# Kernel optimization log

Measured on AMD Instinct MI355X. Metric: run time of the kernel, lower is better.

The kernel has to match this reference:

```python
import jax, jax.numpy as jnp
import numpy as np


def _mlp2(x, W1, b1, W2, b2):
    # Linear -> (BN=identity in eval) -> ReLU -> Linear  (on_last=False: no act on last)
    return jax.nn.relu(x @ W1 + b1) @ W2 + b2


def _layer(x, ef, row, col, pos, p):
    N, Dn = x.shape
    E, De = ef.shape
    (qW, qB, kW, kB, vW, vB, dW1, dB1, dW2, dB2, eW1, eB1, eW2, eB2,
     attW1, attB1, attW2, attB2, nW1, nB1, nW2, nB2, aW, aB) = p
    d_ep = attW2.shape[0]
    H = De // d_ep
    temp = jnp.sqrt(jnp.asarray(d_ep, x.dtype))
    # ---- reverse-edge lookup: for edge (i,j), find edge (j,i) if present ----
    keys = row.astype(jnp.int64) * N + col.astype(jnp.int64)
    rkeys = col.astype(jnp.int64) * N + row.astype(jnp.int64)
    order = jnp.argsort(keys)
    sk = keys[order]
    loc = jnp.clip(jnp.searchsorted(sk, rkeys), 0, E - 1)
    found = sk[loc] == rkeys
    rev = jnp.where(found[:, None], ef[order[loc]], 0.0)  # [E, De]
    # ---- distance mask ----
    diff = pos[row] - pos[col]                              # [E,3]
    dist = jnp.linalg.norm(diff, axis=1, keepdims=True)     # [E,1]
    dfeat = jnp.concatenate([diff, dist], axis=1)           # [E,4]
    dm = jax.nn.sigmoid(_mlp2(dfeat, dW1, dB1, dW2, dB2))[:, 0]  # [E]
    # ---- message ----
    x_i = x[row]
    x_j = x[col]
    upd_edge = _mlp2(jnp.concatenate([x_i, ef, rev, x_j], axis=1), eW1, eB1, eW2, eB2)  # [E,De]
    q = (x_i @ qW + qB).reshape(E, Dn // H, H)              # [E, d_np, H]
    k = (ef @ kW + kB).reshape(E, d_ep, H)                  # [E, d_ep, H]
    v = x_j @ vW + vB                                       # [E, Da]
    h = jnp.concatenate([q, k], axis=1)                     # [E, d_np+d_ep, H]
    h1 = jax.nn.relu(jnp.einsum('ech,oc->eoh', h, attW1) + attB1[None, :, None])
    att = jnp.einsum('ech,oc->eoh', h1, attW2) + attB2[None, :, None]  # [E, d_ep, H]
    att = att * dm[:, None, None]
    prob = jax.nn.softmax(att / temp, axis=1)               # softmax over channel dim
    wv = prob.reshape(E, -1) * v                            # [E, Da]
    # ---- aggregate (scatter max over source node) ----
    agg = jax.ops.segment_max(wv, row, num_segments=N)
    agg = jnp.where(jnp.isneginf(agg), 0.0, agg)
    # ---- node update ----
    upd_node = _mlp2(jnp.concatenate([x, agg], axis=1), nW1, nB1, nW2, nB2)  # [N,Dn]
    # ---- twin-edge attention (mean of updated edges over out/in edges) ----
    ones = jnp.ones((E,), x.dtype)
    dout = jnp.maximum(jax.ops.segment_sum(ones, row, num_segments=N), 1.0)
    din = jnp.maximum(jax.ops.segment_sum(ones, col, num_segments=N), 1.0)
    outf = jax.ops.segment_sum(upd_edge, row, num_segments=N) / dout[:, None]
    incf = jax.ops.segment_sum(upd_edge, col, num_segments=N) / din[:, None]
    eatt = jax.nn.sigmoid(jnp.concatenate([outf, incf], axis=1) @ aW + aB)  # [N,De]
    final = jax.nn.relu(upd_node) * eatt
    return final, upd_edge, prob


def setup_inputs() -> dict:
    N, E, Dn, De, Da, H, L = 10000, 160000, 128, 128, 128, 8, 2
    d_np, d_ep = Dn // H, De // H
    rng = np.random.default_rng(0)
    half = E // 2
    r = rng.integers(0, N, half)
    c = rng.integers(0, N, half)
    edges = jnp.asarray(np.stack([np.concatenate([r, c]), np.concatenate([c, r])]), dtype=jnp.int32)
    ks = iter(jax.random.split(jax.random.key(0), 40))
    def p(*shape, s=0.02):
        return jax.random.normal(next(ks), shape, jnp.float32) * s
    return dict(
        node_feature=p(N, Dn, s=1.0),
        edge_feature=p(E, De, s=1.0),
        edges_indices=edges,
        descriptor=p(N, 8, s=1.0),
        qW=p(L, Dn, Dn), qB=p(L, Dn),
        kW=p(L, De, De), kB=p(L, De),
        vW=p(L, Dn, Da), vB=p(L, Da),
        dW1=p(L, 4, 32), dB1=p(L, 32),
        dW2=p(L, 32, 1), dB2=p(L, 1),
        eW1=p(L, 2 * Dn + 2 * De, Dn + 2 * De), eB1=p(L, Dn + 2 * De),
        eW2=p(L, Dn + 2 * De, De), eB2=p(L, De),
        attW1=p(L, d_np + d_ep, d_np + d_ep), attB1=p(L, d_np + d_ep),
        attW2=p(L, d_ep, d_np + d_ep), attB2=p(L, d_ep),
        nW1=p(L, Dn + Da, Dn + De), nB1=p(L, Dn + De),
        nW2=p(L, Dn + De, Dn), nB2=p(L, Dn),
        aW=p(L, 2 * De, De), aB=p(L, De),
    )


def reference(node_feature, edge_feature, edges_indices, descriptor,
              qW, qB, kW, kB, vW, vB, dW1, dB1, dW2, dB2,
              eW1, eB1, eW2, eB2, attW1, attB1, attW2, attB2,
              nW1, nB1, nW2, nB2, aW, aB):
    row, col = edges_indices[0], edges_indices[1]
    pos = descriptor[:, :3]
    L = qW.shape[0]
    x, ef = node_feature, edge_feature
    probs = []
    for l in range(L):
        p = (qW[l], qB[l], kW[l], kB[l], vW[l], vB[l], dW1[l], dB1[l], dW2[l], dB2[l],
             eW1[l], eB1[l], eW2[l], eB2[l], attW1[l], attB1[l], attW2[l], attB2[l],
             nW1[l], nB1[l], nW2[l], nB2[l], aW[l], aB[l])
        x, ef, prob = _layer(x, ef, row, col, pos, p)
        if l < L - 1 or L == 1:
            x = jax.nn.relu(x)
            ef = jax.nn.relu(ef)
        probs.append(prob)
    return x, ef, jnp.stack(probs)
```

## Files before the change

kernel.cpp:

```cpp
#include <hip/hip_runtime.h>
#include <math.h>

#define HS 524288
#define HSM (HS - 1)
#define ENC_NEGINF 0x007FFFFFu

__device__ __forceinline__ unsigned encf(float f) {
    unsigned b = __float_as_uint(f);
    return (b & 0x80000000u) ? ~b : (b | 0x80000000u);
}
__device__ __forceinline__ float decf(unsigned u) {
    return __uint_as_float((u & 0x80000000u) ? (u & 0x7FFFFFFFu) : ~u);
}

__device__ __forceinline__ unsigned short f2bf(float x) {
    unsigned u = __float_as_uint(x);
    unsigned r = u + 0x7FFFu + ((u >> 16) & 1u);
    return (unsigned short)(r >> 16);
}
__device__ __forceinline__ float bf2f(unsigned short h) {
    return __uint_as_float(((unsigned)h) << 16);
}


__global__ __launch_bounds__(256) void k_init_static(unsigned* hashK, int* hashV,
                                                     int* rowcnt, int* colcnt, int N) {
    int i = blockIdx.x * 256 + threadIdx.x;
    if (i < HS) { hashK[i] = 0xFFFFFFFFu; hashV[i] = 0x7FFFFFFF; }
    if (i < N) { rowcnt[i] = 0; colcnt[i] = 0; }
}

__global__ __launch_bounds__(256) void k_hash_insert(const int* __restrict__ row,
                                                     const int* __restrict__ col,
                                                     unsigned* hashK, int* hashV, int N, int E) {
    int e = blockIdx.x * 256 + threadIdx.x;
    if (e >= E) return;
    unsigned key = (unsigned)row[e] * (unsigned)N + (unsigned)col[e];
    unsigned h = (key * 2654435761u) >> 13; h &= HSM;
    while (true) {
        unsigned prev = atomicCAS(&hashK[h], 0xFFFFFFFFu, key);
        if (prev == 0xFFFFFFFFu || prev == key) { atomicMin(&hashV[h], e); break; }
        h = (h + 1) & HSM;
    }
}

__global__ __launch_bounds__(256) void k_hash_lookup(const int* __restrict__ row,
                                                     const int* __restrict__ col,
                                                     const unsigned* __restrict__ hashK,
                                                     const int* __restrict__ hashV,
                                                     int* __restrict__ ridx,
                                                     int* rowcnt, int* colcnt, int N, int E) {
    int e = blockIdx.x * 256 + threadIdx.x;
    if (e >= E) return;
    int r = row[e], c = col[e];
    unsigned rkey = (unsigned)c * (unsigned)N + (unsigned)r;
    unsigned h = (rkey * 2654435761u) >> 13; h &= HSM;
    int res = -1;
    while (true) {
        unsigned kk = hashK[h];
        if (kk == rkey) { res = hashV[h]; break; }
        if (kk == 0xFFFFFFFFu) break;
        h = (h + 1) & HSM;
    }
    ridx[e] = res;
    atomicAdd(&rowcnt[r], 1);
    atomicAdd(&colcnt[c], 1);
}

__global__ __launch_bounds__(256) void k_layer_init(unsigned* aggenc, float* outf, float* incf, int NC) {
    int i = blockIdx.x * 256 + threadIdx.x;
    if (i >= NC) return;
    aggenc[i] = ENC_NEGINF;
    outf[i] = 0.f;
    incf[i] = 0.f;
}

__global__ __launch_bounds__(256) void k_prep_wt(const float* __restrict__ src,
                                                 unsigned short* __restrict__ whi,
                                                 unsigned short* __restrict__ wlo,
                                                 int K, int Nn) {
    int idx = blockIdx.x * 256 + threadIdx.x;
    if (idx >= K * Nn) return;
    int k = idx / Nn, n = idx - k * Nn;
    float v = src[idx];
    unsigned short h = f2bf(v);
    float hf = bf2f(h);
    unsigned short l = f2bf(v - hf);
    whi[(size_t)n * K + k] = h;
    wlo[(size_t)n * K + k] = l;
}

template <int ACT>
__global__ __launch_bounds__(256) void k_gemm(const float* __restrict__ A,
                                              const float* __restrict__ B,
                                              const float* __restrict__ bias,
                                              float* __restrict__ C,
                                              int M, int Nd, int K, int lda, int ldb, int ldc) {
    __shared__ float As[16][64];
    __shared__ float Bs[16][64];
    const int tid = threadIdx.x;
    const int bm = blockIdx.y * 64, bn = blockIdx.x * 64;
    const int tx = tid & 15, ty = tid >> 4;
    const int mload = tid >> 2, k4 = (tid & 3) << 2;
    const int kload = tid >> 4, n4 = (tid & 15) << 2;
    float acc[4][4] = {};
    const int gmload = bm + mload;
    const bool avalid = (gmload < M);
    const float* aptr = A + (size_t)(avalid ? gmload : (M - 1)) * lda + k4;
    const float* bptr = B + (size_t)kload * ldb + bn + n4;
    for (int kb = 0; kb < K; kb += 16) {
        float4 av = avalid ? *(const float4*)(aptr + kb) : make_float4(0.f, 0.f, 0.f, 0.f);
        As[k4 + 0][mload] = av.x; As[k4 + 1][mload] = av.y;
        As[k4 + 2][mload] = av.z; As[k4 + 3][mload] = av.w;
        *(float4*)&Bs[kload][n4] = *(const float4*)(bptr + (size_t)kb * ldb);
        __syncthreads();
#pragma unroll
        for (int k = 0; k < 16; ++k) {
            float4 a = *(const float4*)&As[k][ty << 2];
            float4 b = *(const float4*)&Bs[k][tx << 2];
            acc[0][0] += a.x * b.x; acc[0][1] += a.x * b.y; acc[0][2] += a.x * b.z; acc[0][3] += a.x * b.w;
            acc[1][0] += a.y * b.x; acc[1][1] += a.y * b.y; acc[1][2] += a.y * b.z; acc[1][3] += a.y * b.w;
            acc[2][0] += a.z * b.x; acc[2][1] += a.z * b.y; acc[2][2] += a.z * b.z; acc[2][3] += a.z * b.w;
            acc[3][0] += a.w * b.x; acc[3][1] += a.w * b.y; acc[3][2] += a.w * b.z; acc[3][3] += a.w * b.w;
        }
        __syncthreads();
    }
#pragma unroll
    for (int i = 0; i < 4; ++i) {
        int gm = bm + (ty << 2) + i;
        if (gm >= M) continue;
        float* crow = C + (size_t)gm * ldc;
#pragma unroll
        for (int j = 0; j < 4; ++j) {
            int gn = bn + (tx << 2) + j;
            float v = acc[i][j];
            if (bias) v += bias[gn];
            if (ACT == 1) v = fmaxf(v, 0.f);
            if (ACT == 2) v = 1.f / (1.f + __expf(-v));
            crow[gn] = v;
        }
    }
}


#define LDP 40

using bfrag = __attribute__((ext_vector_type(8))) short;
using ffrag = __attribute__((ext_vector_type(4))) float;

template <int MODE, int KSTEPS>
__global__ __launch_bounds__(256) void k_mfma_gemm(const float* __restrict__ Asrc,
                                                   const int* __restrict__ ridx,
                                                   const unsigned short* __restrict__ Bhi,
                                                   const unsigned short* __restrict__ Blo,
                                                   const float* __restrict__ bias,
                                                   const float* __restrict__ xa,
                                                   const float* __restrict__ xb,
                                                   const int* __restrict__ rowArr,
                                                   const int* __restrict__ colArr,
                                                   float* __restrict__ outC,
                                                   float* __restrict__ outf,
                                                   float* __restrict__ incf,
                                                   int edgeBase, int Mrows, int reluOut) {
    constexpr int K = KSTEPS * 32;
    __shared__ unsigned short Ah[128 * LDP];
    __shared__ unsigned short Al[128 * LDP];
    __shared__ unsigned short Bh[128 * LDP];
    __shared__ unsigned short Bl[128 * LDP];

    const int tid = threadIdx.x;
    const int bm = blockIdx.y * 128;
    const int bx = blockIdx.x;

    const int sr = tid >> 1;
    const int kh = (tid & 1) * 16;

    const float* p0;
    const float* p1 = nullptr;
    {
        int rc = min(bm + sr, Mrows - 1);
        if (MODE == 0) {
            int e = edgeBase + rc;
            p0 = Asrc + (size_t)e * 128;
            int rv = ridx[e];
            p1 = (rv >= 0) ? (Asrc + (size_t)rv * 128) : nullptr;
        } else if (MODE == 1) {
            p0 = Asrc + (size_t)rc * 384;
        } else {
            p0 = Asrc + (size_t)rc * 128;
        }
    }
    const unsigned short* bhp = Bhi + (size_t)(bx * 128 + sr) * K + kh;
    const unsigned short* blp = Blo + (size_t)(bx * 128 + sr) * K + kh;

    const int wid = tid >> 6;
    const int lane = tid & 63;
    const int wr0 = (wid >> 1) * 64;
    const int wc0 = (wid & 1) * 64;
    const int lm = lane & 15;
    const int lk = (lane >> 4) * 8;

    ffrag acc[4][4];
#pragma unroll
    for (int i = 0; i < 4; ++i)
#pragma unroll
        for (int j = 0; j < 4; ++j)
            acc[i][j] = (ffrag){0.f, 0.f, 0.f, 0.f};

    unsigned short* AhW = &Ah[sr * LDP + kh];
    unsigned short* AlW = &Al[sr * LDP + kh];
    unsigned short* BhW = &Bh[sr * LDP + kh];
    unsigned short* BlW = &Bl[sr * LDP + kh];

    for (int ks = 0; ks < KSTEPS; ++ks) {
        const int kb = ks * 32;
        const float* ap;
        if (MODE == 0) ap = (kb < 128) ? (p0 + kb) : (p1 ? p1 + (kb - 128) : nullptr);
        else ap = p0 + kb;
#pragma unroll
        for (int c = 0; c < 4; ++c) {
            float4 f = ap ? *(const float4*)(ap + kh + c * 4) : make_float4(0.f, 0.f, 0.f, 0.f);
            ushort4 h, l;
            h.x = f2bf(f.x); l.x = f2bf(f.x - bf2f(h.x));
            h.y = f2bf(f.y); l.y = f2bf(f.y - bf2f(h.y));
            h.z = f2bf(f.z); l.z = f2bf(f.z - bf2f(h.z));
            h.w = f2bf(f.w); l.w = f2bf(f.w - bf2f(h.w));
            *(ushort4*)(AhW + c * 4) = h;
            *(ushort4*)(AlW + c * 4) = l;
        }
        {
            uint4 b0 = *(const uint4*)(bhp + kb);
            uint4 b1 = *(const uint4*)(bhp + kb + 8);
            uint4 c0 = *(const uint4*)(blp + kb);
            uint4 c1 = *(const uint4*)(blp + kb + 8);
            *(uint4*)(BhW) = b0; *(uint4*)(BhW + 8) = b1;
            *(uint4*)(BlW) = c0; *(uint4*)(BlW + 8) = c1;
        }
        __syncthreads();
        bfrag a_h[4], a_l[4], b_h[4], b_l[4];
#pragma unroll
        for (int mt = 0; mt < 4; ++mt) {
            int base = (wr0 + mt * 16 + lm) * LDP + lk;
            a_h[mt] = *(const bfrag*)&Ah[base];
            a_l[mt] = *(const bfrag*)&Al[base];
        }
#pragma unroll
        for (int nt = 0; nt < 4; ++nt) {
            int base = (wc0 + nt * 16 + lm) * LDP + lk;
            b_h[nt] = *(const bfrag*)&Bh[base];
            b_l[nt] = *(const bfrag*)&Bl[base];
        }
#pragma unroll
        for (int mt = 0; mt < 4; ++mt)
#pragma unroll
            for (int nt = 0; nt < 4; ++nt) {
                acc[mt][nt] = __builtin_amdgcn_mfma_f32_16x16x32_bf16(a_h[mt], b_h[nt], acc[mt][nt], 0, 0, 0);
                acc[mt][nt] = __builtin_amdgcn_mfma_f32_16x16x32_bf16(a_l[mt], b_h[nt], acc[mt][nt], 0, 0, 0);
                acc[mt][nt] = __builtin_amdgcn_mfma_f32_16x16x32_bf16(a_h[mt], b_l[nt], acc[mt][nt], 0, 0, 0);
            }
        __syncthreads();
    }

    float bv[4];
#pragma unroll
    for (int nt = 0; nt < 4; ++nt) bv[nt] = bias[bx * 128 + wc0 + nt * 16 + lm];

#pragma unroll
    for (int mt = 0; mt < 4; ++mt) {
#pragma unroll
        for (int i = 0; i < 4; ++i) {
            int grow = bm + wr0 + mt * 16 + (lane >> 4) * 4 + i;
            if (grow >= Mrows) continue;
            if (MODE == 0) {
                int e = edgeBase + grow;
                size_t re = (size_t)rowArr[e] * 384;
                size_t ce = (size_t)colArr[e] * 384;
                float* crow = outC + (size_t)grow * 384;
#pragma unroll
                for (int nt = 0; nt < 4; ++nt) {
                    int gcol = bx * 128 + wc0 + nt * 16 + lm;
                    float v = acc[mt][nt][i] + bv[nt] + xa[re + gcol] + xb[ce + gcol];
                    crow[gcol] = fmaxf(v, 0.f);
                }
            } else if (MODE == 1) {
                int e = edgeBase + grow;
                size_t re = (size_t)rowArr[e] * 128;
                size_t ce = (size_t)colArr[e] * 128;
                float* crow = outC + (size_t)e * 128;
#pragma unroll
                for (int nt = 0; nt < 4; ++nt) {
                    int gcol = wc0 + nt * 16 + lm;
                    float v = acc[mt][nt][i] + bv[nt];
                    atomicAdd(&outf[re + gcol], v);
                    atomicAdd(&incf[ce + gcol], v);
                    crow[gcol] = reluOut ? fmaxf(v, 0.f) : v;
                }
            } else {
                float* crow = outC + (size_t)grow * 128;
#pragma unroll
                for (int nt = 0; nt < 4; ++nt) {
                    int gcol = wc0 + nt * 16 + lm;
                    crow[gcol] = acc[mt][nt][i] + bv[nt];
                }
            }
        }
    }
}


__global__ __launch_bounds__(256) void k_attn(const float* __restrict__ xq,
                                              const float* __restrict__ kbuf,
                                              const float* __restrict__ xv,
                                              const float* __restrict__ desc,
                                              const int* __restrict__ row,
                                              const int* __restrict__ col,
                                              const float* __restrict__ attW1,
                                              const float* __restrict__ attB1,
                                              const float* __restrict__ attW2,
                                              const float* __restrict__ attB2,
                                              const float* __restrict__ dW1,
                                              const float* __restrict__ dB1,
                                              const float* __restrict__ dW2,
                                              const float* __restrict__ dB2,
                                              float* __restrict__ prob_out,
                                              unsigned* __restrict__ aggenc, int E) {
    __shared__ float w1t[32 * 36];
    __shared__ float w2t[32 * 18];
    __shared__ float sdw1[128];
    __shared__ float sQ[4][128];
    __shared__ float sK[4][128];
    __shared__ float sV[4][128];
    __shared__ float sP[4][128];
    for (int i = threadIdx.x; i < 1024; i += 256) {
        int o = i >> 5, c = i & 31;
        w1t[c * 36 + o] = attW1[i];
    }
    for (int i = threadIdx.x; i < 512; i += 256) {
        int o = i >> 5, c = i & 31;
        w2t[c * 18 + o] = attW2[i];
    }
    for (int i = threadIdx.x; i < 128; i += 256) sdw1[i] = dW1[i];
    __syncthreads();

    const int wv = threadIdx.x >> 6;
    const int lane = threadIdx.x & 63;
    const int hd = lane & 7;
    const int og = lane >> 3;
    const int c32 = lane & 31;
    const int nw = (gridDim.x * 256) >> 6;
    const int wid = (blockIdx.x * 256 + threadIdx.x) >> 6;

    float* myQ = sQ[wv];
    float* myK = sK[wv];
    float* myV = sV[wv];
    float* myP = sP[wv];

    const float b1_0 = attB1[og * 4 + 0], b1_1 = attB1[og * 4 + 1];
    const float b1_2 = attB1[og * 4 + 2], b1_3 = attB1[og * 4 + 3];
    const float b2_0 = attB2[og * 2 + 0], b2_1 = attB2[og * 2 + 1];
    const float db2v = dB2[0];
    const float dw2v = dW2[c32];
    const float db1v = dB1[c32];

    for (int e0 = wid; e0 < E; e0 += nw) {
        const int e = __builtin_amdgcn_readfirstlane(e0);
        const int r = row[e], cl = col[e];
        float2 qv = *(const float2*)(xq + (size_t)r * 128 + lane * 2);
        float2 kv = *(const float2*)(kbuf + (size_t)e * 128 + lane * 2);
        float2 vv = *(const float2*)(xv + (size_t)cl * 128 + lane * 2);
        *(float2*)(myQ + lane * 2) = qv;
        *(float2*)(myK + lane * 2) = kv;
        *(float2*)(myV + lane * 2) = vv;
        __builtin_amdgcn_wave_barrier();

        float dx = desc[r * 8 + 0] - desc[cl * 8 + 0];
        float dy = desc[r * 8 + 1] - desc[cl * 8 + 1];
        float dz = desc[r * 8 + 2] - desc[cl * 8 + 2];
        float dist = sqrtf(dx * dx + dy * dy + dz * dz);
        float t = db1v + dx * sdw1[c32] + dy * sdw1[32 + c32] + dz * sdw1[64 + c32] + dist * sdw1[96 + c32];
        t = fmaxf(t, 0.f) * dw2v;
        t += __shfl_xor(t, 1, 64); t += __shfl_xor(t, 2, 64); t += __shfl_xor(t, 4, 64);
        t += __shfl_xor(t, 8, 64); t += __shfl_xor(t, 16, 64);
        float dm = 1.f / (1.f + __expf(-(t + db2v)));

        float h0 = b1_0, h1v = b1_1, h2 = b1_2, h3 = b1_3;
#pragma unroll
        for (int ci = 0; ci < 16; ++ci) {
            float hv = myQ[ci * 8 + hd];
            const float4 w = *(const float4*)&w1t[ci * 36 + og * 4];
            h0 += hv * w.x; h1v += hv * w.y; h2 += hv * w.z; h3 += hv * w.w;
        }
#pragma unroll
        for (int ci = 0; ci < 16; ++ci) {
            float hv = myK[ci * 8 + hd];
            const float4 w = *(const float4*)&w1t[(16 + ci) * 36 + og * 4];
            h0 += hv * w.x; h1v += hv * w.y; h2 += hv * w.z; h3 += hv * w.w;
        }
        float hreg[4];
        hreg[0] = fmaxf(h0, 0.f); hreg[1] = fmaxf(h1v, 0.f);
        hreg[2] = fmaxf(h2, 0.f); hreg[3] = fmaxf(h3, 0.f);

        float a0 = b2_0, a1 = b2_1;
#pragma unroll
        for (int c = 0; c < 32; ++c) {
            int src = (c >> 2) * 8 + hd;
            float hv = __shfl(hreg[c & 3], src, 64);
            const float2 w = *(const float2*)&w2t[c * 18 + og * 2];
            a0 += hv * w.x; a1 += hv * w.y;
        }
        float sc = dm * 0.25f;
        a0 *= sc; a1 *= sc;

        float mx = fmaxf(a0, a1);
        mx = fmaxf(mx, __shfl_xor(mx, 8, 64));
        mx = fmaxf(mx, __shfl_xor(mx, 16, 64));
        mx = fmaxf(mx, __shfl_xor(mx, 32, 64));
        float e0v = __expf(a0 - mx), e1v = __expf(a1 - mx);
        float s = e0v + e1v;
        s += __shfl_xor(s, 8, 64); s += __shfl_xor(s, 16, 64); s += __shfl_xor(s, 32, 64);
        float inv = 1.f / s;
        float p0 = e0v * inv, p1 = e1v * inv;

        myP[og * 16 + hd] = p0;
        myP[og * 16 + hd + 8] = p1;

        float v0 = myV[og * 16 + hd] * p0;
        float v1 = myV[og * 16 + hd + 8] * p1;
        unsigned* ab = aggenc + (size_t)r * 128 + og * 16 + hd;
        atomicMax(ab, encf(v0));
        atomicMax(ab + 8, encf(v1));

        __builtin_amdgcn_wave_barrier();
        *(float2*)(prob_out + (size_t)e * 128 + lane * 2) = *(const float2*)(myP + lane * 2);
    }
}


__global__ __launch_bounds__(256) void k_ncat(const float* __restrict__ x,
                                              const unsigned* __restrict__ aggenc,
                                              float* __restrict__ ncat, int N) {
    int i = blockIdx.x * 256 + threadIdx.x;
    if (i >= N * 256) return;
    int n = i >> 8, c = i & 255;
    float v;
    if (c < 128) v = x[n * 128 + c];
    else {
        unsigned u = aggenc[n * 128 + c - 128];
        v = (u == ENC_NEGINF) ? 0.f : decf(u);
    }
    ncat[i] = v;
}

__global__ __launch_bounds__(256) void k_cat2(const float* __restrict__ outf,
                                              const float* __restrict__ incf,
                                              const int* __restrict__ rowcnt,
                                              const int* __restrict__ colcnt,
                                              float* __restrict__ cat2, int N) {
    int i = blockIdx.x * 256 + threadIdx.x;
    if (i >= N * 256) return;
    int n = i >> 8, c = i & 255;
    float v;
    if (c < 128) v = outf[n * 128 + c] / fmaxf((float)rowcnt[n], 1.f);
    else v = incf[n * 128 + c - 128] / fmaxf((float)colcnt[n], 1.f);
    cat2[i] = v;
}

__global__ __launch_bounds__(256) void k_final(const float* __restrict__ un,
                                               const float* __restrict__ eatt,
                                               float* __restrict__ dst, int NC) {
    int i = blockIdx.x * 256 + threadIdx.x;
    if (i >= NC) return;
    dst[i] = fmaxf(un[i], 0.f) * eatt[i];
}


extern "C" void kernel_launch(void* const* d_in, const int* in_sizes, int n_in,
                              void* d_out, int out_size, void* d_ws, size_t ws_size,
                              hipStream_t stream) {
    const float* node_feature = (const float*)d_in[0];
    const float* edge_feature = (const float*)d_in[1];
    const int* edges = (const int*)d_in[2];
    const float* desc = (const float*)d_in[3];
    const float* qW = (const float*)d_in[4];
    const float* qB = (const float*)d_in[5];
    const float* kW = (const float*)d_in[6];
    const float* kB = (const float*)d_in[7];
    const float* vW = (const float*)d_in[8];
    const float* vB = (const float*)d_in[9];
    const float* dW1 = (const float*)d_in[10];
    const float* dB1 = (const float*)d_in[11];
    const float* dW2 = (const float*)d_in[12];
    const float* dB2 = (const float*)d_in[13];
    const float* eW1 = (const float*)d_in[14];
    const float* eB1 = (const float*)d_in[15];
    const float* eW2 = (const float*)d_in[16];
    const float* eB2 = (const float*)d_in[17];
    const float* attW1 = (const float*)d_in[18];
    const float* attB1 = (const float*)d_in[19];
    const float* attW2 = (const float*)d_in[20];
    const float* attB2 = (const float*)d_in[21];
    const float* nW1 = (const float*)d_in[22];
    const float* nB1 = (const float*)d_in[23];
    const float* nW2 = (const float*)d_in[24];
    const float* nB2 = (const float*)d_in[25];
    const float* aW = (const float*)d_in[26];
    const float* aB = (const float*)d_in[27];

    const int N = in_sizes[0] / 128;
    const int E = in_sizes[2] / 2;
    const int L = 2;
    const int* row = edges;
    const int* col = edges + E;

    char* wsp = (char*)d_ws;
    auto alloc = [&](size_t bytes) {
        char* p = wsp;
        wsp += (bytes + 255) & ~(size_t)255;
        return p;
    };
    unsigned* hashK = (unsigned*)alloc((size_t)HS * 4);
    int* hashV = (int*)alloc((size_t)HS * 4);
    int* ridx = (int*)alloc((size_t)E * 4);
    int* rowcnt = (int*)alloc((size_t)N * 4);
    int* colcnt = (int*)alloc((size_t)N * 4);
    float* xq = (float*)alloc((size_t)N * 128 * 4);
    float* xv = (float*)alloc((size_t)N * 128 * 4);
    float* xa = (float*)alloc((size_t)N * 384 * 4);
    float* xb = (float*)alloc((size_t)N * 384 * 4);
    float* kbuf = (float*)alloc((size_t)E * 128 * 4);
    float* efbuf = (float*)alloc((size_t)E * 128 * 4);
    const int CH = 32000;
    float* h1c = (float*)alloc((size_t)CH * 384 * 4);
    unsigned* aggenc = (unsigned*)alloc((size_t)N * 128 * 4);
    float* ncat = (float*)alloc((size_t)N * 256 * 4);
    float* nh1 = (float*)alloc((size_t)N * 256 * 4);
    float* un = (float*)alloc((size_t)N * 128 * 4);
    float* outf = (float*)alloc((size_t)N * 128 * 4);
    float* incf = (float*)alloc((size_t)N * 128 * 4);
    float* cat2 = (float*)alloc((size_t)N * 256 * 4);
    float* eattb = (float*)alloc((size_t)N * 128 * 4);
    float* xbuf = (float*)alloc((size_t)N * 128 * 4);
    unsigned short* wt1_hi = (unsigned short*)alloc((size_t)384 * 256 * 2);
    unsigned short* wt1_lo = (unsigned short*)alloc((size_t)384 * 256 * 2);
    unsigned short* wt2_hi = (unsigned short*)alloc((size_t)128 * 384 * 2);
    unsigned short* wt2_lo = (unsigned short*)alloc((size_t)128 * 384 * 2);
    unsigned short* wtk_hi = (unsigned short*)alloc((size_t)128 * 128 * 2);
    unsigned short* wtk_lo = (unsigned short*)alloc((size_t)128 * 128 * 2);

    float* out_x = (float*)d_out;
    float* out_ef = out_x + (size_t)N * 128;
    float* out_prob = out_ef + (size_t)E * 128;

    k_init_static<<<(HS + 255) / 256, 256, 0, stream>>>(hashK, hashV, rowcnt, colcnt, N);
    k_hash_insert<<<(E + 255) / 256, 256, 0, stream>>>(row, col, hashK, hashV, N, E);
    k_hash_lookup<<<(E + 255) / 256, 256, 0, stream>>>(row, col, hashK, hashV, ridx, rowcnt, colcnt, N, E);

    for (int l = 0; l < L; ++l) {
        const float* x_cur = (l == 0) ? node_feature : xbuf;
        const float* ef_cur = (l == 0) ? edge_feature : efbuf;
        const bool last = (l == L - 1);

        const float* qW_l = qW + (size_t)l * 128 * 128;
        const float* qB_l = qB + (size_t)l * 128;
        const float* kW_l = kW + (size_t)l * 128 * 128;
        const float* kB_l = kB + (size_t)l * 128;
        const float* vW_l = vW + (size_t)l * 128 * 128;
        const float* vB_l = vB + (size_t)l * 128;
        const float* dW1_l = dW1 + (size_t)l * 128;
        const float* dB1_l = dB1 + (size_t)l * 32;
        const float* dW2_l = dW2 + (size_t)l * 32;
        const float* dB2_l = dB2 + (size_t)l * 1;
        const float* eW1_l = eW1 + (size_t)l * 512 * 384;
        const float* eB1_l = eB1 + (size_t)l * 384;
        const float* eW2_l = eW2 + (size_t)l * 384 * 128;
        const float* eB2_l = eB2 + (size_t)l * 128;
        const float* attW1_l = attW1 + (size_t)l * 32 * 32;
        const float* attB1_l = attB1 + (size_t)l * 32;
        const float* attW2_l = attW2 + (size_t)l * 16 * 32;
        const float* attB2_l = attB2 + (size_t)l * 16;
        const float* nW1_l = nW1 + (size_t)l * 256 * 256;
        const float* nB1_l = nB1 + (size_t)l * 256;
        const float* nW2_l = nW2 + (size_t)l * 256 * 128;
        const float* nB2_l = nB2 + (size_t)l * 128;
        const float* aW_l = aW + (size_t)l * 256 * 128;
        const float* aB_l = aB + (size_t)l * 128;

        k_prep_wt<<<(256 * 384 + 255) / 256, 256, 0, stream>>>(eW1_l + (size_t)128 * 384, wt1_hi, wt1_lo, 256, 384);
        k_prep_wt<<<(384 * 128 + 255) / 256, 256, 0, stream>>>(eW2_l, wt2_hi, wt2_lo, 384, 128);
        k_prep_wt<<<(128 * 128 + 255) / 256, 256, 0, stream>>>(kW_l, wtk_hi, wtk_lo, 128, 128);

        k_layer_init<<<(N * 128 + 255) / 256, 256, 0, stream>>>(aggenc, outf, incf, N * 128);

        int gy_n = (N + 63) / 64;
        k_gemm<0><<<dim3(2, gy_n), 256, 0, stream>>>(x_cur, qW_l, qB_l, xq, N, 128, 128, 128, 128, 128);
        k_gemm<0><<<dim3(2, gy_n), 256, 0, stream>>>(x_cur, vW_l, vB_l, xv, N, 128, 128, 128, 128, 128);
        k_gemm<0><<<dim3(6, gy_n), 256, 0, stream>>>(x_cur, eW1_l, nullptr, xa, N, 384, 128, 128, 384, 384);
        k_gemm<0><<<dim3(6, gy_n), 256, 0, stream>>>(x_cur, eW1_l + (size_t)384 * 384, nullptr, xb, N, 384, 128, 128, 384, 384);
        k_mfma_gemm<2, 4><<<dim3(1, (E + 127) / 128), 256, 0, stream>>>(
            ef_cur, nullptr, wtk_hi, wtk_lo, kB_l, nullptr, nullptr, nullptr, nullptr,
            kbuf, nullptr, nullptr, 0, E, 0);
        k_attn<<<4096, 256, 0, stream>>>(xq, kbuf, xv, desc, row, col, attW1_l, attB1_l, attW2_l, attB2_l,
                                         dW1_l, dB1_l, dW2_l, dB2_l,
                                         out_prob + (size_t)l * E * 128, aggenc, E);
        for (int cb = 0; cb < E; cb += CH) {
            int mrows = (E - cb < CH) ? (E - cb) : CH;
            int gy = (mrows + 127) / 128;
            k_mfma_gemm<0, 8><<<dim3(3, gy), 256, 0, stream>>>(
                ef_cur, ridx, wt1_hi, wt1_lo, eB1_l, xa, xb, row, col,
                h1c, nullptr, nullptr, cb, mrows, 0);
            k_mfma_gemm<1, 12><<<dim3(1, gy), 256, 0, stream>>>(
                h1c, nullptr, wt2_hi, wt2_lo, eB2_l, nullptr, nullptr, row, col,
                last ? out_ef : efbuf, outf, incf, cb, mrows, last ? 0 : 1);
        }
        k_ncat<<<(N * 256 + 255) / 256, 256, 0, stream>>>(x_cur, aggenc, ncat, N);
        k_gemm<1><<<dim3(4, gy_n), 256, 0, stream>>>(ncat, nW1_l, nB1_l, nh1, N, 256, 256, 256, 256, 256);
        k_gemm<0><<<dim3(2, gy_n), 256, 0, stream>>>(nh1, nW2_l, nB2_l, un, N, 128, 256, 256, 128, 128);
        k_cat2<<<(N * 256 + 255) / 256, 256, 0, stream>>>(outf, incf, rowcnt, colcnt, cat2, N);
        k_gemm<2><<<dim3(2, gy_n), 256, 0, stream>>>(cat2, aW_l, aB_l, eattb, N, 128, 256, 256, 128, 128);
        k_final<<<(N * 128 + 255) / 256, 256, 0, stream>>>(un, eattb, last ? out_x : xbuf, N * 128);
    }
}
```

Baseline: 2.382 ms.

## Remap attention to one edge-head per lane and split distance mask kernel

The attention kernel now gives each lane one (edge, head) pair, eight edges per wave, and computes the two small MLPs fully in registers with weights in shared memory. This replaces the old one-edge-per-wave mapping that staged data in LDS and used many cross-lane shuffles. The distance-mask MLP moves into its own per-edge kernel that writes a buffer, which adds a launch and an extra pass over the edges. The new mapping uses many more registers per thread and makes strided 4-byte gathers for q, k, v and the prob stores.

```diff
diff --git a/kernel.cpp b/kernel.cpp
--- a/kernel.cpp
+++ b/kernel.cpp
@@ -308,130 +308,145 @@
 }
 
 
+__global__ __launch_bounds__(256) void k_dm(const float* __restrict__ desc,
+                                            const int* __restrict__ row,
+                                            const int* __restrict__ col,
+                                            const float* __restrict__ dW1,
+                                            const float* __restrict__ dB1,
+                                            const float* __restrict__ dW2,
+                                            const float* __restrict__ dB2,
+                                            float* __restrict__ dmbuf, int E) {
+    __shared__ float sw[128];
+    __shared__ float sb[32];
+    __shared__ float sv[32];
+    for (int i = threadIdx.x; i < 128; i += 256) sw[i] = dW1[i];
+    if (threadIdx.x < 32) { sb[threadIdx.x] = dB1[threadIdx.x]; sv[threadIdx.x] = dW2[threadIdx.x]; }
+    __syncthreads();
+    const float db2v = dB2[0];
+    for (int e = blockIdx.x * 256 + threadIdx.x; e < E; e += gridDim.x * 256) {
+        int r = row[e], c = col[e];
+        float dx = desc[r * 8 + 0] - desc[c * 8 + 0];
+        float dy = desc[r * 8 + 1] - desc[c * 8 + 1];
+        float dz = desc[r * 8 + 2] - desc[c * 8 + 2];
+        float dist = sqrtf(dx * dx + dy * dy + dz * dz);
+        float acc = db2v;
+#pragma unroll
+        for (int j = 0; j < 32; ++j) {
+            float t = sb[j] + dx * sw[j] + dy * sw[32 + j] + dz * sw[64 + j] + dist * sw[96 + j];
+            acc += fmaxf(t, 0.f) * sv[j];
+        }
+        dmbuf[e] = 1.f / (1.f + __expf(-acc));
+    }
+}
+
+
 __global__ __launch_bounds__(256) void k_attn(const float* __restrict__ xq,
                                               const float* __restrict__ kbuf,
                                               const float* __restrict__ xv,
-                                              const float* __restrict__ desc,
                                               const int* __restrict__ row,
                                               const int* __restrict__ col,
                                               const float* __restrict__ attW1,
                                               const float* __restrict__ attB1,
                                               const float* __restrict__ attW2,
                                               const float* __restrict__ attB2,
-                                              const float* __restrict__ dW1,
-                                              const float* __restrict__ dB1,
-                                              const float* __restrict__ dW2,
-                                              const float* __restrict__ dB2,
+                                              const float* __restrict__ dmbuf,
                                               float* __restrict__ prob_out,
                                               unsigned* __restrict__ aggenc, int E) {
-    __shared__ float w1t[32 * 36];
-    __shared__ float w2t[32 * 18];
-    __shared__ float sdw1[128];
-    __shared__ float sQ[4][128];
-    __shared__ float sK[4][128];
-    __shared__ float sV[4][128];
-    __shared__ float sP[4][128];
-    for (int i = threadIdx.x; i < 1024; i += 256) {
-        int o = i >> 5, c = i & 31;
-        w1t[c * 36 + o] = attW1[i];
-    }
-    for (int i = threadIdx.x; i < 512; i += 256) {
-        int o = i >> 5, c = i & 31;
-        w2t[c * 18 + o] = attW2[i];
-    }
-    for (int i = threadIdx.x; i < 128; i += 256) sdw1[i] = dW1[i];
+    __shared__ float sW1[1024];
+    __shared__ float sW2[512];
+    __shared__ float sB1[32];
+    __shared__ float sB2[16];
+    for (int i = threadIdx.x; i < 1024; i += 256) sW1[i] = attW1[i];
+    for (int i = threadIdx.x; i < 512; i += 256) sW2[i] = attW2[i];
+    if (threadIdx.x < 32) sB1[threadIdx.x] = attB1[threadIdx.x];
+    if (threadIdx.x < 16) sB2[threadIdx.x] = attB2[threadIdx.x];
     __syncthreads();
 
-    const int wv = threadIdx.x >> 6;
     const int lane = threadIdx.x & 63;
+    const int le = lane >> 3;
     const int hd = lane & 7;
-    const int og = lane >> 3;
-    const int c32 = lane & 31;
+    const int gwave = (blockIdx.x * 256 + threadIdx.x) >> 6;
     const int nw = (gridDim.x * 256) >> 6;
-    const int wid = (blockIdx.x * 256 + threadIdx.x) >> 6;
-
-    float* myQ = sQ[wv];
-    float* myK = sK[wv];
-    float* myV = sV[wv];
-    float* myP = sP[wv];
-
-    const float b1_0 = attB1[og * 4 + 0], b1_1 = attB1[og * 4 + 1];
-    const float b1_2 = attB1[og * 4 + 2], b1_3 = attB1[og * 4 + 3];
-    const float b2_0 = attB2[og * 2 + 0], b2_1 = attB2[og * 2 + 1];
-    const float db2v = dB2[0];
-    const float dw2v = dW2[c32];
-    const float db1v = dB1[c32];
-
-    for (int e0 = wid; e0 < E; e0 += nw) {
-        const int e = __builtin_amdgcn_readfirstlane(e0);
-        const int r = row[e], cl = col[e];
-        float2 qv = *(const float2*)(xq + (size_t)r * 128 + lane * 2);
-        float2 kv = *(const float2*)(kbuf + (size_t)e * 128 + lane * 2);
-        float2 vv = *(const float2*)(xv + (size_t)cl * 128 + lane * 2);
-        *(float2*)(myQ + lane * 2) = qv;
-        *(float2*)(myK + lane * 2) = kv;
-        *(float2*)(myV + lane * 2) = vv;
-        __builtin_amdgcn_wave_barrier();
-
-        float dx = desc[r * 8 + 0] - desc[cl * 8 + 0];
-        float dy = desc[r * 8 + 1] - desc[cl * 8 + 1];
-        float dz = desc[r * 8 + 2] - desc[cl * 8 + 2];
-        float dist = sqrtf(dx * dx + dy * dy + dz * dz);
-        float t = db1v + dx * sdw1[c32] + dy * sdw1[32 + c32] + dz * sdw1[64 + c32] + dist * sdw1[96 + c32];
-        t = fmaxf(t, 0.f) * dw2v;
-        t += __shfl_xor(t, 1, 64); t += __shfl_xor(t, 2, 64); t += __shfl_xor(t, 4, 64);
-        t += __shfl_xor(t, 8, 64); t += __shfl_xor(t, 16, 64);
-        float dm = 1.f / (1.f + __expf(-(t + db2v)));
-
-        float h0 = b1_0, h1v = b1_1, h2 = b1_2, h3 = b1_3;
-#pragma unroll
-        for (int ci = 0; ci < 16; ++ci) {
-            float hv = myQ[ci * 8 + hd];
-            const float4 w = *(const float4*)&w1t[ci * 36 + og * 4];
-            h0 += hv * w.x; h1v += hv * w.y; h2 += hv * w.z; h3 += hv * w.w;
-        }
-#pragma unroll
-        for (int ci = 0; ci < 16; ++ci) {
-            float hv = myK[ci * 8 + hd];
-            const float4 w = *(const float4*)&w1t[(16 + ci) * 36 + og * 4];
-            h0 += hv * w.x; h1v += hv * w.y; h2 += hv * w.z; h3 += hv * w.w;
-        }
-        float hreg[4];
-        hreg[0] = fmaxf(h0, 0.f); hreg[1] = fmaxf(h1v, 0.f);
-        hreg[2] = fmaxf(h2, 0.f); hreg[3] = fmaxf(h3, 0.f);
-
-        float a0 = b2_0, a1 = b2_1;
-#pragma unroll
-        for (int c = 0; c < 32; ++c) {
-            int src = (c >> 2) * 8 + hd;
-            float hv = __shfl(hreg[c & 3], src, 64);
-            const float2 w = *(const float2*)&w2t[c * 18 + og * 2];
-            a0 += hv * w.x; a1 += hv * w.y;
-        }
-        float sc = dm * 0.25f;
-        a0 *= sc; a1 *= sc;
-
-        float mx = fmaxf(a0, a1);
-        mx = fmaxf(mx, __shfl_xor(mx, 8, 64));
-        mx = fmaxf(mx, __shfl_xor(mx, 16, 64));
-        mx = fmaxf(mx, __shfl_xor(mx, 32, 64));
-        float e0v = __expf(a0 - mx), e1v = __expf(a1 - mx);
-        float s = e0v + e1v;
-        s += __shfl_xor(s, 8, 64); s += __shfl_xor(s, 16, 64); s += __shfl_xor(s, 32, 64);
-        float inv = 1.f / s;
-        float p0 = e0v * inv, p1 = e1v * inv;
-
-        myP[og * 16 + hd] = p0;
-        myP[og * 16 + hd + 8] = p1;
-
-        float v0 = myV[og * 16 + hd] * p0;
-        float v1 = myV[og * 16 + hd + 8] * p1;
-        unsigned* ab = aggenc + (size_t)r * 128 + og * 16 + hd;
-        atomicMax(ab, encf(v0));
-        atomicMax(ab + 8, encf(v1));
-
-        __builtin_amdgcn_wave_barrier();
-        *(float2*)(prob_out + (size_t)e * 128 + lane * 2) = *(const float2*)(myP + lane * 2);
+    const int ngrp = (E + 7) >> 3;
+
+    for (int g = gwave; g < ngrp; g += nw) {
+        const int e = g * 8 + le;
+        const bool valid = (e < E);
+        const int ec = valid ? e : (E - 1);
+        const int r = row[ec], cl = col[ec];
+        const float dm = dmbuf[ec];
+
+        float h[32];
+        const float* qp = xq + (size_t)r * 128 + hd;
+        const float* kp = kbuf + (size_t)ec * 128 + hd;
+#pragma unroll
+        for (int ci = 0; ci < 16; ++ci) h[ci] = qp[ci * 8];
+#pragma unroll
+        for (int ci = 0; ci < 16; ++ci) h[16 + ci] = kp[ci * 8];
+
+        float h1[32];
+#pragma unroll
+        for (int o = 0; o < 32; o += 4) {
+            float a0 = sB1[o], a1 = sB1[o + 1], a2 = sB1[o + 2], a3 = sB1[o + 3];
+#pragma unroll
+            for (int c = 0; c < 32; c += 4) {
+                float4 w0 = *(const float4*)&sW1[(o    ) * 32 + c];
+                float4 w1 = *(const float4*)&sW1[(o + 1) * 32 + c];
+                float4 w2 = *(const float4*)&sW1[(o + 2) * 32 + c];
+                float4 w3 = *(const float4*)&sW1[(o + 3) * 32 + c];
+                float x0 = h[c], x1 = h[c + 1], x2 = h[c + 2], x3 = h[c + 3];
+                a0 += x0 * w0.x + x1 * w0.y + x2 * w0.z + x3 * w0.w;
+                a1 += x0 * w1.x + x1 * w1.y + x2 * w1.z + x3 * w1.w;
+                a2 += x0 * w2.x + x1 * w2.y + x2 * w2.z + x3 * w2.w;
+                a3 += x0 * w3.x + x1 * w3.y + x2 * w3.z + x3 * w3.w;
+            }
+            h1[o] = fmaxf(a0, 0.f); h1[o + 1] = fmaxf(a1, 0.f);
+            h1[o + 2] = fmaxf(a2, 0.f); h1[o + 3] = fmaxf(a3, 0.f);
+        }
+
+        float att[16];
+#pragma unroll
+        for (int o = 0; o < 16; o += 4) {
+            float a0 = sB2[o], a1 = sB2[o + 1], a2 = sB2[o + 2], a3 = sB2[o + 3];
+#pragma unroll
+            for (int c = 0; c < 32; c += 4) {
+                float4 w0 = *(const float4*)&sW2[(o    ) * 32 + c];
+                float4 w1 = *(const float4*)&sW2[(o + 1) * 32 + c];
+                float4 w2 = *(const float4*)&sW2[(o + 2) * 32 + c];
+                float4 w3 = *(const float4*)&sW2[(o + 3) * 32 + c];
+                float x0 = h1[c], x1 = h1[c + 1], x2 = h1[c + 2], x3 = h1[c + 3];
+                a0 += x0 * w0.x + x1 * w0.y + x2 * w0.z + x3 * w0.w;
+                a1 += x0 * w1.x + x1 * w1.y + x2 * w1.z + x3 * w1.w;
+                a2 += x0 * w2.x + x1 * w2.y + x2 * w2.z + x3 * w2.w;
+                a3 += x0 * w3.x + x1 * w3.y + x2 * w3.z + x3 * w3.w;
+            }
+            att[o] = a0; att[o + 1] = a1; att[o + 2] = a2; att[o + 3] = a3;
+        }
+
+        const float sc = dm * 0.25f;
+#pragma unroll
+        for (int i = 0; i < 16; ++i) att[i] *= sc;
+        float mx = att[0];
+#pragma unroll
+        for (int i = 1; i < 16; ++i) mx = fmaxf(mx, att[i]);
+        float s = 0.f;
+        float p[16];
+#pragma unroll
+        for (int i = 0; i < 16; ++i) { p[i] = __expf(att[i] - mx); s += p[i]; }
+        const float inv = 1.f / s;
+
+        if (valid) {
+            float* pr = prob_out + (size_t)e * 128 + hd;
+            const float* vp = xv + (size_t)cl * 128 + hd;
+            unsigned* ab = aggenc + (size_t)r * 128 + hd;
+#pragma unroll
+            for (int o2 = 0; o2 < 16; ++o2) {
+                float pi = p[o2] * inv;
+                pr[o2 * 8] = pi;
+                float wv = pi * vp[o2 * 8];
+                atomicMax(ab + o2 * 8, encf(wv));
+            }
+        }
     }
 }
 
@@ -529,6 +544,7 @@
     float* xb = (float*)alloc((size_t)N * 384 * 4);
     float* kbuf = (float*)alloc((size_t)E * 128 * 4);
     float* efbuf = (float*)alloc((size_t)E * 128 * 4);
+    float* dmbuf = (float*)alloc((size_t)E * 4);
     const int CH = 32000;
     float* h1c = (float*)alloc((size_t)CH * 384 * 4);
     unsigned* aggenc = (unsigned*)alloc((size_t)N * 128 * 4);
@@ -591,6 +607,8 @@
 
         k_layer_init<<<(N * 128 + 255) / 256, 256, 0, stream>>>(aggenc, outf, incf, N * 128);
 
+        k_dm<<<(E + 255) / 256, 256, 0, stream>>>(desc, row, col, dW1_l, dB1_l, dW2_l, dB2_l, dmbuf, E);
+
         int gy_n = (N + 63) / 64;
         k_gemm<0><<<dim3(2, gy_n), 256, 0, stream>>>(x_cur, qW_l, qB_l, xq, N, 128, 128, 128, 128, 128);
         k_gemm<0><<<dim3(2, gy_n), 256, 0, stream>>>(x_cur, vW_l, vB_l, xv, N, 128, 128, 128, 128, 128);
@@ -599,9 +617,8 @@
         k_mfma_gemm<2, 4><<<dim3(1, (E + 127) / 128), 256, 0, stream>>>(
             ef_cur, nullptr, wtk_hi, wtk_lo, kB_l, nullptr, nullptr, nullptr, nullptr,
             kbuf, nullptr, nullptr, 0, E, 0);
-        k_attn<<<4096, 256, 0, stream>>>(xq, kbuf, xv, desc, row, col, attW1_l, attB1_l, attW2_l, attB2_l,
-                                         dW1_l, dB1_l, dW2_l, dB2_l,
-                                         out_prob + (size_t)l * E * 128, aggenc, E);
+        k_attn<<<2048, 256, 0, stream>>>(xq, kbuf, xv, row, col, attW1_l, attB1_l, attW2_l, attB2_l,
+                                         dmbuf, out_prob + (size_t)l * E * 128, aggenc, E);
         for (int cb = 0; cb < E; cb += CH) {
             int mrows = (E - cb < CH) ? (E - cb) : CH;
             int gy = (mrows + 127) / 128;
```

Result: slower. 2.859 ms (+20.0%).
